# Kernel tuning notes

Hardware: AMD Instinct MI355X
Metric: run time of the kernel (lower is better)

Reference implementation:

```python
import jax, jax.numpy as jnp
import numpy as np

B, S, M, E, H, F, V, L = 2, 2048, 1024, 512, 8, 2048, 8192, 6


def setup_inputs() -> dict:
    key = jax.random.key(0)
    ks = iter(jax.random.split(key, 32))
    n = lambda shape, s=0.02: jax.random.normal(next(ks), shape, jnp.float32) * s
    return {
        "encoded": jax.random.normal(next(ks), (B, M, E), jnp.float32),
        "seq": jax.random.randint(next(ks), (B, S), 0, V, jnp.int32),
        "input_embed": n((V, E)),           # shared input/output embedding
        "pos_embed": n((S, E)),
        "output_bias": jnp.zeros((V,), jnp.float32),
        "self_in_w": n((L, 3 * E, E)), "self_in_b": jnp.zeros((L, 3 * E), jnp.float32),
        "self_out_w": n((L, E, E)), "self_out_b": jnp.zeros((L, E), jnp.float32),
        "cross_in_w": n((L, 3 * E, E)), "cross_in_b": jnp.zeros((L, 3 * E), jnp.float32),
        "cross_out_w": n((L, E, E)), "cross_out_b": jnp.zeros((L, E), jnp.float32),
        "self_norm_g": jnp.ones((L, E), jnp.float32), "self_norm_b": jnp.zeros((L, E), jnp.float32),
        "cross_norm_g": jnp.ones((L, E), jnp.float32), "cross_norm_b": jnp.zeros((L, E), jnp.float32),
        "mlp_norm_g": jnp.ones((L, E), jnp.float32), "mlp_norm_b": jnp.zeros((L, E), jnp.float32),
        "lin1_w": n((L, F, E)), "lin1_b": jnp.zeros((L, F), jnp.float32),
        "lin2_w": n((L, E, F)), "lin2_b": jnp.zeros((L, E), jnp.float32),
        "final_norm_g": jnp.ones((E,), jnp.float32), "final_norm_b": jnp.zeros((E,), jnp.float32),
    }


def _ln(x, g, b, eps=1e-5):
    m = jnp.mean(x, axis=-1, keepdims=True)
    v = jnp.mean((x - m) ** 2, axis=-1, keepdims=True)
    return (x - m) * jax.lax.rsqrt(v + eps) * g + b


def _mha(q, k, v, in_w, in_b, out_w, out_b, mask):
    # torch nn.MultiheadAttention (batch_first) with packed in_proj [3E, E]
    Ed = q.shape[-1]
    dh = Ed // H
    qp = q @ in_w[:Ed].T + in_b[:Ed]
    kp = k @ in_w[Ed:2 * Ed].T + in_b[Ed:2 * Ed]
    vp = v @ in_w[2 * Ed:].T + in_b[2 * Ed:]
    split = lambda t: t.reshape(t.shape[0], t.shape[1], H, dh).transpose(0, 2, 1, 3)
    qh, kh, vh = split(qp), split(kp), split(vp)  # [B, H, S, dh]
    scores = jnp.einsum('bhqd,bhkd->bhqk', qh, kh) / jnp.sqrt(jnp.float32(dh))
    if mask is not None:
        scores = jnp.where(mask, scores, jnp.float32(-1e9))
    attn = jax.nn.softmax(scores, axis=-1)
    o = jnp.einsum('bhqk,bhkd->bhqd', attn, vh)
    o = o.transpose(0, 2, 1, 3).reshape(q.shape[0], q.shape[1], Ed)
    return o @ out_w.T + out_b


def reference(encoded, seq, input_embed, pos_embed, output_bias,
              self_in_w, self_in_b, self_out_w, self_out_b,
              cross_in_w, cross_in_b, cross_out_w, cross_out_b,
              self_norm_g, self_norm_b, cross_norm_g, cross_norm_b,
              mlp_norm_g, mlp_norm_b, lin1_w, lin1_b, lin2_w, lin2_b,
              final_norm_g, final_norm_b):
    # TransformerDecoder.fit: teacher-forced forward (eval-mode dropout = identity)
    seq_len = seq.shape[1]
    x = input_embed[seq] + pos_embed[:seq_len]          # [B, S, E]
    causal = jnp.tril(jnp.ones((seq_len, seq_len), bool))
    for i in range(L):
        # post-norm decoder layer (norm_first=False)
        attn = _mha(x, x, x, self_in_w[i], self_in_b[i], self_out_w[i], self_out_b[i], causal)
        y = _ln(x + attn, self_norm_g[i], self_norm_b[i])
        cattn = _mha(y, encoded, encoded, cross_in_w[i], cross_in_b[i], cross_out_w[i], cross_out_b[i], None)
        y = _ln(y + cattn, cross_norm_g[i], cross_norm_b[i])
        h = jax.nn.gelu(y @ lin1_w[i].T + lin1_b[i], approximate=False)
        x = _ln(y + h @ lin2_w[i].T + lin2_b[i], mlp_norm_g[i], mlp_norm_b[i])
    x = _ln(x, final_norm_g, final_norm_b)               # decoder-final norm
    return x @ input_embed.T + output_bias               # shared output embedding
```

## Files before the change

### kernel.cpp

```cpp
#include <hip/hip_runtime.h>
#include <math.h>

typedef unsigned short u16;
typedef __attribute__((ext_vector_type(8))) unsigned short u16x8;
typedef __attribute__((ext_vector_type(8))) __bf16 bf16x8;
typedef __attribute__((ext_vector_type(4))) float f32x4;

constexpr int Bc = 2, Sc = 2048, Mc = 1024, Ec = 512, Hc = 8, DH = 64, Fc = 2048, Vc = 8192, Lc = 6;
constexpr int Nc = Bc * Sc;
constexpr int NMc = Bc * Mc;

__device__ __forceinline__ u16 f2b(float f) {
  __bf16 h = (__bf16)f;
  return __builtin_bit_cast(u16, h);
}
__device__ __forceinline__ float b2f_lo(unsigned w) { return __builtin_bit_cast(float, w << 16); }
__device__ __forceinline__ float b2f_hi(unsigned w) { return __builtin_bit_cast(float, w & 0xFFFF0000u); }

__device__ __forceinline__ f32x4 mfma16(bf16x8 a, bf16x8 b, f32x4 c) {
  return __builtin_amdgcn_mfma_f32_16x16x32_bf16(a, b, c, 0, 0, 0);
}

constexpr int C0 = 1179648;
constexpr int C1 = C0 + 393216;
constexpr int C2 = C1 + 1179648;
constexpr int C3 = C2 + 393216;
constexpr int C4 = C3 + 1572864;
constexpr int C5 = C4 + 1572864;
constexpr int C6 = C5 + 1048576;
constexpr int C7 = C6 + 262144;
constexpr int C8 = C7 + Nc * Ec / 4;

__global__ __launch_bounds__(256) void k_cvt_all(
    const float* __restrict__ s0, const float* __restrict__ s1,
    const float* __restrict__ s2, const float* __restrict__ s3,
    const float* __restrict__ s4, const float* __restrict__ s5,
    const float* __restrict__ s6, const float* __restrict__ s7,
    u16* __restrict__ d0, u16* __restrict__ d1, u16* __restrict__ d2,
    u16* __restrict__ d3, u16* __restrict__ d4, u16* __restrict__ d5,
    u16* __restrict__ d6, u16* __restrict__ d7,
    const int* __restrict__ seq, const float* __restrict__ pos,
    float* __restrict__ xs, u16* __restrict__ xb) {
  int i = blockIdx.x * 256 + threadIdx.x;
  if (i >= C7) {
    int j = i - C7;
    int idx0 = j * 4;
    int row = idx0 >> 9, e = idx0 & 511;
    int s = row & (Sc - 1);
    float4 ev = *(const float4*)(s6 + (size_t)seq[row] * Ec + e);
    float4 pv = *(const float4*)(pos + (size_t)s * Ec + e);
    float4 v = make_float4(ev.x + pv.x, ev.y + pv.y, ev.z + pv.z, ev.w + pv.w);
    ((float4*)xs)[j] = v;
    unsigned lo = (unsigned)f2b(v.x) | ((unsigned)f2b(v.y) << 16);
    unsigned hi = (unsigned)f2b(v.z) | ((unsigned)f2b(v.w) << 16);
    ((uint2*)xb)[j] = make_uint2(lo, hi);
    return;
  }
  const float* s; u16* d; int off;
  if (i < C3) {
    if (i < C1) { if (i < C0) { s = s0; d = d0; off = i; }
                  else        { s = s1; d = d1; off = i - C0; } }
    else        { if (i < C2) { s = s2; d = d2; off = i - C1; }
                  else        { s = s3; d = d3; off = i - C2; } }
  } else {
    if (i < C5) { if (i < C4) { s = s4; d = d4; off = i - C3; }
                  else        { s = s5; d = d5; off = i - C4; } }
    else        { if (i < C6) { s = s6; d = d6; off = i - C5; }
                  else        { s = s7; d = d7; off = i - C6; } }
  }
  float4 v = ((const float4*)s)[off];
  unsigned lo = (unsigned)f2b(v.x) | ((unsigned)f2b(v.y) << 16);
  unsigned hi = (unsigned)f2b(v.z) | ((unsigned)f2b(v.w) << 16);
  ((uint2*)d)[off] = make_uint2(lo, hi);
}

template <int BM, int BN, int ACT>
__device__ __forceinline__ void gemm_body(const u16* __restrict__ A,
                                          const u16* __restrict__ W,
                                          const float* __restrict__ bias,
                                          float* __restrict__ C32,
                                          u16* __restrict__ Cb,
                                          int K, int Mo,
                                          size_t row0, size_t col0) {
  constexpr int WM = BM / 2, WN = BN / 2, FM = WM / 16, FN = WN / 16;
  __shared__ __attribute__((aligned(16))) u16 As[2][BM * 64];
  __shared__ __attribute__((aligned(16))) u16 Bs[2][BN * 64];
  const int tid = threadIdx.x;
  const int w = tid >> 6, l = tid & 63, l15 = l & 15, l4 = l >> 4;
  const int lr = l >> 3, lc = l & 7;
  const int wr = (w >> 1) * WM, wc = (w & 1) * WN;
  const u16* Ab = A + row0 * K;
  const u16* Wb = W + col0 * K;
  f32x4 acc[FM][FN] = {};

  auto stage = [&](int buf, int k0) {
#pragma unroll
    for (int i = 0; i < BM / 32; ++i) {
      int sw = lr ^ ((i * 4 + w) & 7);
      int row = i * 32 + w * 8 + lr;
      const u16* ga = Ab + (size_t)row * K + k0 + ((lc ^ sw) & 7) * 8;
      __builtin_amdgcn_global_load_lds((const __attribute__((address_space(1))) void*)ga,
          (__attribute__((address_space(3))) void*)((char*)As[buf] + (i * 32 + w * 8) * 128), 16, 0, 0);
    }
#pragma unroll
    for (int i = 0; i < BN / 32; ++i) {
      int sw = lr ^ ((i * 4 + w) & 7);
      int row = i * 32 + w * 8 + lr;
      const u16* gw = Wb + (size_t)row * K + k0 + ((lc ^ sw) & 7) * 8;
      __builtin_amdgcn_global_load_lds((const __attribute__((address_space(1))) void*)gw,
          (__attribute__((address_space(3))) void*)((char*)Bs[buf] + (i * 32 + w * 8) * 128), 16, 0, 0);
    }
  };
  auto compute = [&](int buf) {
    const u16* AsC = As[buf];
    const u16* BsC = Bs[buf];
#pragma unroll
    for (int ks = 0; ks < 2; ++ks) {
      bf16x8 af[FM], bfr[FN];
#pragma unroll
      for (int m = 0; m < FM; ++m) {
        int ra = wr + m * 16 + l15;
        int sw = (l15 & 7) ^ ((wr / 8 + 2 * m + (l15 >> 3)) & 7);
        af[m] = *(const bf16x8*)&AsC[ra * 64 + ((ks * 32 + l4 * 8) ^ (sw * 8))];
      }
#pragma unroll
      for (int n = 0; n < FN; ++n) {
        int rb = wc + n * 16 + l15;
        int sw = (l15 & 7) ^ ((wc / 8 + 2 * n + (l15 >> 3)) & 7);
        bfr[n] = *(const bf16x8*)&BsC[rb * 64 + ((ks * 32 + l4 * 8) ^ (sw * 8))];
      }
#pragma unroll
      for (int m = 0; m < FM; ++m)
#pragma unroll
        for (int n = 0; n < FN; ++n)
          acc[m][n] = mfma16(af[m], bfr[n], acc[m][n]);
    }
  };

  const int nk = K / 64;
  stage(0, 0);
  int cur = 0;
  for (int kt = 0; kt < nk; ++kt) {
    __syncthreads();
    if (kt + 1 < nk) stage(cur ^ 1, (kt + 1) * 64);
    compute(cur);
    cur ^= 1;
  }

#pragma unroll
  for (int n = 0; n < FN; ++n) {
    size_t col = col0 + wc + n * 16 + l15;
    float bv = bias[col];
#pragma unroll
    for (int m = 0; m < FM; ++m)
#pragma unroll
      for (int r = 0; r < 4; ++r) {
        size_t row = row0 + wr + m * 16 + l4 * 4 + r;
        float v = acc[m][n][r] + bv;
        if (ACT) v = 0.5f * v * (1.f + erff(v * 0.70710678118654752f));
        if (C32) C32[row * Mo + col] = v;
        if (Cb) Cb[row * Mo + col] = f2b(v);
      }
  }
}

template <int BM, int BN, int ACT, int XS>
__global__ __launch_bounds__(256) void k_gemm_bf(const u16* __restrict__ A,
                                                 const u16* __restrict__ W,
                                                 const float* __restrict__ bias,
                                                 float* __restrict__ C32,
                                                 u16* __restrict__ Cb,
                                                 int K, int Mo) {
  int bx, by;
  if constexpr (XS) {
    int gx = gridDim.x;
    int bid = blockIdx.x + gx * blockIdx.y;
    int cw = gx >> 3;
    int xcd = bid & 7, j = bid >> 3;
    bx = xcd * cw + (j % cw);
    by = j / cw;
  } else {
    bx = blockIdx.x; by = blockIdx.y;
  }
  gemm_body<BM, BN, ACT>(A, W, bias, C32, Cb, K, Mo, (size_t)by * BM, (size_t)bx * BN);
}

__global__ __launch_bounds__(256) void k_gemm_cross(
    const u16* __restrict__ A0, const u16* __restrict__ W0, const float* __restrict__ b0,
    u16* __restrict__ Co0,
    const u16* __restrict__ A1, const u16* __restrict__ W1, const float* __restrict__ b1,
    u16* __restrict__ Co1) {
  int bid = blockIdx.x;
  if (bid < 512) {
    int xcd = bid & 7, j = bid >> 3;
    gemm_body<64, 64, 0>(A0, W0, b0, nullptr, Co0, Ec, Ec, (size_t)j * 64, (size_t)xcd * 64);
  } else {
    int r = bid - 512;
    int xcd = r & 7, j = r >> 3;
    int bx = xcd * 2 + (j & 1), by = j >> 1;
    gemm_body<64, 64, 0>(A1, W1, b1, nullptr, Co1, Ec, 2 * Ec, (size_t)by * 64, (size_t)bx * 64);
  }
}

__global__ __launch_bounds__(512, 4) void k_flash(const u16* __restrict__ Qp, int sq,
                                                  const u16* __restrict__ Kp,
                                                  const u16* __restrict__ Vp, int skv,
                                                  u16* __restrict__ Op, int so,
                                                  int Sq, int Sk, int causal) {
  __shared__ __attribute__((aligned(16))) u16 Kst[4][64 * 64];
  __shared__ __attribute__((aligned(16))) u16 Vt[4][64 * 64];
  __shared__ __attribute__((aligned(16))) u16 Pl[8][16 * 64];
  const int tid = threadIdx.x;
  const int w = tid >> 6, l = tid & 63, l15 = l & 15, l4 = l >> 4;
  const int wq = w & 3, ws = w >> 2;
  const int lr = l >> 3, lc = l & 7;
  const int t256 = tid & 255;
  const int kk2 = t256 >> 3, dblk = tid & 7;
  const int nqt = Sq / 64, nkt = Sk / 64;
  const int h = blockIdx.y, b = blockIdx.z;
  const int bx = blockIdx.x;
  const int qi = causal ? ((b & 1) ? bx : (nqt - 1 - bx)) : bx;
  const int qt0 = qi * 64;
  const int nt = causal ? (qi + 1) : nkt;
  const int NI = (nt + 1) >> 1;
  const u16* Qb = Qp + (size_t)b * Sq * sq + h * DH;
  const u16* Kb = Kp + (size_t)b * Sk * skv + h * DH;
  const u16* Vb = Vp + (size_t)b * Sk * skv + h * DH;
  const int qg = qt0 + wq * 16 + l15;

  bf16x8 qf[2];
  {
    const u16* qp0 = Qb + (size_t)qg * sq + l4 * 8;
    qf[0] = *(const bf16x8*)(qp0);
    qf[1] = *(const bf16x8*)(qp0 + 32);
  }

  f32x4 oacc[4] = {};
  float ls = 0.f, Mx = -3e38f;
  const float CSC = 0.18033688011112042f;
  const int swp = (l15 & 7) ^ (l15 >> 3);

  u16x8 va, vbv;
  auto stageK = [&](int slot, int kt) {
#pragma unroll
    for (int i = 0; i < 2; ++i) {
      int sw = lr ^ ((i * 4 + wq) & 7);
      int row = i * 32 + wq * 8 + lr;
      const u16* src = Kb + (size_t)(kt + row) * skv + ((lc ^ sw) & 7) * 8;
      __builtin_amdgcn_global_load_lds((const __attribute__((address_space(1))) void*)src,
          (__attribute__((address_space(3))) void*)((char*)Kst[slot] + (i * 32 + wq * 8) * 128), 16, 0, 0);
    }
  };
  auto loadV = [&](int kt) {
    const u16* vp0 = Vb + (size_t)(kt + 2 * kk2) * skv + dblk * 8;
    va = *(const u16x8*)vp0;
    vbv = *(const u16x8*)(vp0 + skv);
  };
  auto writeV = [&](int slot) {
    char* Vb_ = (char*)Vt[slot];
#pragma unroll
    for (int j = 0; j < 8; ++j) {
      int d = dblk * 8 + j;
      int sw = (j ^ dblk) & 7;
      unsigned pk = (unsigned)va[j] | ((unsigned)vbv[j] << 16);
      *(unsigned*)(Vb_ + d * 128 + ((4 * kk2) ^ (sw << 4))) = pk;
    }
  };

  stageK(ws * 2, ws * 64);
  loadV(ws * 64);
  writeV(ws * 2);
  asm volatile("s_waitcnt lgkmcnt(0)" ::: "memory");
  __builtin_amdgcn_sched_barrier(0);
  __builtin_amdgcn_s_barrier();

  u16* Pw = Pl[w];
  for (int i = 0; i < NI; ++i) {
    const int t = 2 * i + ws;
    const int tn = t + 2;
    const int cur = ws * 2 + (i & 1);
    const int nxt = ws * 2 + ((i + 1) & 1);
    const bool haveNext = tn < nt;
    if (haveNext) {
      stageK(nxt, tn * 64);
      loadV(tn * 64);
    }
    if (t < nt) {
      const u16* KstC = Kst[cur];
      const u16* VtC = Vt[cur];

      f32x4 sf[4] = {};
      __builtin_amdgcn_s_setprio(1);
#pragma unroll
      for (int n = 0; n < 4; ++n) {
        int rk = n * 16 + l15;
        int sw = (l15 & 7) ^ ((2 * n + (l15 >> 3)) & 7);
#pragma unroll
        for (int ks = 0; ks < 2; ++ks) {
          bf16x8 kf = *(const bf16x8*)&KstC[rk * 64 + ((ks * 32 + l4 * 8) ^ (sw * 8))];
          sf[n] = mfma16(kf, qf[ks], sf[n]);
        }
      }
      __builtin_amdgcn_s_setprio(0);

      if (causal && t == nt - 1) {
#pragma unroll
        for (int n = 0; n < 4; ++n)
#pragma unroll
          for (int r = 0; r < 4; ++r) {
            int kcol = t * 64 + n * 16 + l4 * 4 + r;
            if (kcol > qg) sf[n][r] = -3e38f;
          }
      }

      float tm = fmaxf(fmaxf(fmaxf(sf[0][0], sf[0][1]), fmaxf(sf[0][2], sf[0][3])),
                       fmaxf(fmaxf(sf[1][0], sf[1][1]), fmaxf(sf[1][2], sf[1][3])));
      tm = fmaxf(tm, fmaxf(fmaxf(fmaxf(sf[2][0], sf[2][1]), fmaxf(sf[2][2], sf[2][3])),
                           fmaxf(fmaxf(sf[3][0], sf[3][1]), fmaxf(sf[3][2], sf[3][3]))));
      tm = fmaxf(tm, __shfl_xor(tm, 16, 64));
      tm = fmaxf(tm, __shfl_xor(tm, 32, 64));
      float Mn = fmaxf(Mx, tm);
      float al = exp2f((Mx - Mn) * CSC);
      Mx = Mn;
      float mxc = Mx * CSC;

      float rs = 0.f;
#pragma unroll
      for (int n = 0; n < 4; ++n) {
        float p0 = exp2f(sf[n][0] * CSC - mxc);
        float p1 = exp2f(sf[n][1] * CSC - mxc);
        float p2 = exp2f(sf[n][2] * CSC - mxc);
        float p3 = exp2f(sf[n][3] * CSC - mxc);
        rs += (p0 + p1) + (p2 + p3);
        unsigned w0 = (unsigned)f2b(p0) | ((unsigned)f2b(p1) << 16);
        unsigned w1 = (unsigned)f2b(p2) | ((unsigned)f2b(p3) << 16);
        int bb = (n * 32 + l4 * 8) ^ (swp << 4);
        *(unsigned*)((char*)Pw + l15 * 128 + bb) = w0;
        *(unsigned*)((char*)Pw + l15 * 128 + bb + 4) = w1;
      }
      rs += __shfl_xor(rs, 16, 64);
      rs += __shfl_xor(rs, 32, 64);
      ls = ls * al + rs;

      if (__any(al < 1.f)) {
        float a0 = __shfl(al, l4 * 4 + 0, 64);
        float a1 = __shfl(al, l4 * 4 + 1, 64);
        float a2 = __shfl(al, l4 * 4 + 2, 64);
        float a3 = __shfl(al, l4 * 4 + 3, 64);
#pragma unroll
        for (int n2 = 0; n2 < 4; ++n2) {
          oacc[n2][0] *= a0; oacc[n2][1] *= a1;
          oacc[n2][2] *= a2; oacc[n2][3] *= a3;
        }
      }

      asm volatile("s_waitcnt lgkmcnt(0)" ::: "memory");
      __builtin_amdgcn_sched_barrier(0);

      __builtin_amdgcn_s_setprio(1);
#pragma unroll
      for (int ks = 0; ks < 2; ++ks) {
        bf16x8 pf = *(const bf16x8*)((char*)Pw + l15 * 128 + ((ks * 64 + l4 * 16) ^ (swp << 4)));
#pragma unroll
        for (int n2 = 0; n2 < 4; ++n2) {
          int rd = n2 * 16 + l15;
          int sw = (l15 & 7) ^ ((2 * n2 + (l15 >> 3)) & 7);
          bf16x8 vf = *(const bf16x8*)((char*)VtC + rd * 128 + ((ks * 64 + l4 * 16) ^ (sw << 4)));
          oacc[n2] = mfma16(pf, vf, oacc[n2]);
        }
      }
      __builtin_amdgcn_s_setprio(0);
    }

    if (haveNext) writeV(nxt);
    asm volatile("s_waitcnt lgkmcnt(0)" ::: "memory");
    __builtin_amdgcn_sched_barrier(0);
    __builtin_amdgcn_s_barrier();
  }

  __syncthreads();
  float* OB = (float*)&Kst[0][0];
  float* ML = (float*)&Vt[0][0];
  if (l4 == 0) {
    ML[ws * 64 + wq * 16 + l15] = Mx;
    ML[128 + ws * 64 + wq * 16 + l15] = ls;
  }
  if (ws == 1) {
#pragma unroll
    for (int n2 = 0; n2 < 4; ++n2)
#pragma unroll
      for (int r = 0; r < 4; ++r)
        OB[(wq * 16 + l4 * 4 + r) * 64 + n2 * 16 + l15] = oacc[n2][r];
  }
  __syncthreads();
  if (ws == 0) {
    u16* Ob = Op + (size_t)b * Sq * so + h * DH;
#pragma unroll
    for (int r = 0; r < 4; ++r) {
      int qs = wq * 16 + l4 * 4 + r;
      float mA = ML[qs], mB = ML[64 + qs];
      float lA = ML[128 + qs], lB = ML[192 + qs];
      float M = fmaxf(mA, mB);
      float aA = exp2f((mA - M) * CSC);
      float aB = exp2f((mB - M) * CSC);
      float inv = 1.f / (lA * aA + lB * aB);
      int qrow = qt0 + qs;
#pragma unroll
      for (int n2 = 0; n2 < 4; ++n2) {
        float o = (oacc[n2][r] * aA + OB[qs * 64 + n2 * 16 + l15] * aB) * inv;
        Ob[(size_t)qrow * so + n2 * 16 + l15] = f2b(o);
      }
    }
  }
}

__global__ __launch_bounds__(256) void k_res_ln(const float* __restrict__ xin,
                                                const u16* __restrict__ rres,
                                                const float* __restrict__ g,
                                                const float* __restrict__ bet,
                                                float* __restrict__ outf,
                                                u16* __restrict__ outb,
                                                int has_res) {
  const int tid = threadIdx.x, w = tid >> 6, l = tid & 63;
  const int row = blockIdx.x * 4 + w;
  const float4* xr = (const float4*)(xin + (size_t)row * Ec);
  float4 a = xr[2 * l], c = xr[2 * l + 1];
  if (has_res) {
    uint4 rv = ((const uint4*)(rres + (size_t)row * Ec))[l];
    a.x += b2f_lo(rv.x); a.y += b2f_hi(rv.x);
    a.z += b2f_lo(rv.y); a.w += b2f_hi(rv.y);
    c.x += b2f_lo(rv.z); c.y += b2f_hi(rv.z);
    c.z += b2f_lo(rv.w); c.w += b2f_hi(rv.w);
  }
  float s = (a.x + a.y) + (a.z + a.w) + (c.x + c.y) + (c.z + c.w);
#pragma unroll
  for (int o = 32; o; o >>= 1) s += __shfl_xor(s, o, 64);
  const float mean = s * (1.f / Ec);
  float d0 = a.x - mean, d1 = a.y - mean, d2 = a.z - mean, d3 = a.w - mean;
  float e0 = c.x - mean, e1 = c.y - mean, e2 = c.z - mean, e3 = c.w - mean;
  float vs = d0 * d0 + d1 * d1 + d2 * d2 + d3 * d3 +
             e0 * e0 + e1 * e1 + e2 * e2 + e3 * e3;
#pragma unroll
  for (int o = 32; o; o >>= 1) vs += __shfl_xor(vs, o, 64);
  const float inv = rsqrtf(vs * (1.f / Ec) + 1e-5f);
  float4 g0 = ((const float4*)g)[2 * l], g1 = ((const float4*)g)[2 * l + 1];
  float4 b0 = ((const float4*)bet)[2 * l], b1 = ((const float4*)bet)[2 * l + 1];
  float o0 = d0 * inv * g0.x + b0.x, o1 = d1 * inv * g0.y + b0.y;
  float o2 = d2 * inv * g0.z + b0.z, o3 = d3 * inv * g0.w + b0.w;
  float o4 = e0 * inv * g1.x + b1.x, o5 = e1 * inv * g1.y + b1.y;
  float o6 = e2 * inv * g1.z + b1.z, o7 = e3 * inv * g1.w + b1.w;
  if (outf) {
    float4* orow = (float4*)(outf + (size_t)row * Ec);
    orow[2 * l] = make_float4(o0, o1, o2, o3);
    orow[2 * l + 1] = make_float4(o4, o5, o6, o7);
  }
  if (outb) {
    uint4 pk;
    pk.x = (unsigned)f2b(o0) | ((unsigned)f2b(o1) << 16);
    pk.y = (unsigned)f2b(o2) | ((unsigned)f2b(o3) << 16);
    pk.z = (unsigned)f2b(o4) | ((unsigned)f2b(o5) << 16);
    pk.w = (unsigned)f2b(o6) | ((unsigned)f2b(o7) << 16);
    ((uint4*)(outb + (size_t)row * Ec))[l] = pk;
  }
}

extern "C" void kernel_launch(void* const* d_in, const int* in_sizes, int n_in,
                              void* d_out, int out_size, void* d_ws, size_t ws_size,
                              hipStream_t stream) {
  const float* encoded      = (const float*)d_in[0];
  const int*   seq          = (const int*)d_in[1];
  const float* input_embed  = (const float*)d_in[2];
  const float* pos_embed    = (const float*)d_in[3];
  const float* output_bias  = (const float*)d_in[4];
  const float* self_in_w    = (const float*)d_in[5];
  const float* self_in_b    = (const float*)d_in[6];
  const float* self_out_w   = (const float*)d_in[7];
  const float* self_out_b   = (const float*)d_in[8];
  const float* cross_in_w   = (const float*)d_in[9];
  const float* cross_in_b   = (const float*)d_in[10];
  const float* cross_out_w  = (const float*)d_in[11];
  const float* cross_out_b  = (const float*)d_in[12];
  const float* self_norm_g  = (const float*)d_in[13];
  const float* self_norm_b  = (const float*)d_in[14];
  const float* cross_norm_g = (const float*)d_in[15];
  const float* cross_norm_b = (const float*)d_in[16];
  const float* mlp_norm_g   = (const float*)d_in[17];
  const float* mlp_norm_b   = (const float*)d_in[18];
  const float* lin1_w       = (const float*)d_in[19];
  const float* lin1_b       = (const float*)d_in[20];
  const float* lin2_w       = (const float*)d_in[21];
  const float* lin2_b       = (const float*)d_in[22];
  const float* final_norm_g = (const float*)d_in[23];
  const float* final_norm_b = (const float*)d_in[24];

  char* oc = (char*)d_out;
  auto take = [&](size_t bytes) { char* p = oc; oc += bytes; return p; };
  u16* wsi  = (u16*)take((size_t)Lc * 3 * Ec * Ec * 2);
  u16* wso  = (u16*)take((size_t)Lc * Ec * Ec * 2);
  u16* wci  = (u16*)take((size_t)Lc * 3 * Ec * Ec * 2);
  u16* wco  = (u16*)take((size_t)Lc * Ec * Ec * 2);
  u16* wl1  = (u16*)take((size_t)Lc * Fc * Ec * 2);
  u16* wl2  = (u16*)take((size_t)Lc * Ec * Fc * 2);
  u16* encb = (u16*)take((size_t)NMc * Ec * 2);
  float* xs  = (float*)take((size_t)Nc * Ec * 4);
  float* ys  = (float*)take((size_t)Nc * Ec * 4);
  u16* tmpb = (u16*)take((size_t)Nc * Ec * 2);
  u16* xbf  = (u16*)take((size_t)Nc * Ec * 2);
  u16* qkvb = (u16*)take((size_t)Nc * 3 * Ec * 2);
  u16* ctxb = (u16*)take((size_t)Nc * Ec * 2);
  u16* qxb  = (u16*)take((size_t)Nc * Ec * 2);
  u16* kvb  = (u16*)take((size_t)NMc * 2 * Ec * 2);
  u16* hbf  = (u16*)take((size_t)Nc * Fc * 2);
  u16* xfb  = (u16*)d_ws;
  u16* embb = (u16*)((char*)d_ws + (size_t)Nc * Ec * 2);

  const dim3 blk(256);
  k_cvt_all<<<dim3(C8 / 256), blk, 0, stream>>>(
      self_in_w, self_out_w, cross_in_w, cross_out_w, lin1_w, lin2_w,
      input_embed, encoded, wsi, wso, wci, wco, wl1, wl2, embb, encb,
      seq, pos_embed, xs, xbf);

  const dim3 gAttn(Sc / 64, Hc, Bc);
  const dim3 blkA(512);
  const dim3 gLN(Nc / 4);
  for (int l = 0; l < Lc; ++l) {
    const u16* wsi_l = wsi + (size_t)l * 3 * Ec * Ec;
    const u16* wci_l = wci + (size_t)l * 3 * Ec * Ec;
    k_gemm_bf<128, 64, 0, 1><<<dim3(3 * Ec / 64, Nc / 128), blk, 0, stream>>>(
        xbf, wsi_l, self_in_b + (size_t)l * 3 * Ec, nullptr, qkvb, Ec, 3 * Ec);
    k_flash<<<gAttn, blkA, 0, stream>>>(qkvb, 3 * Ec, qkvb + Ec, qkvb + 2 * Ec, 3 * Ec,
                                        ctxb, Ec, Sc, Sc, 1);
    k_gemm_bf<64, 64, 0, 1><<<dim3(Ec / 64, Nc / 64), blk, 0, stream>>>(
        ctxb, wso + (size_t)l * Ec * Ec, self_out_b + (size_t)l * Ec, nullptr, tmpb, Ec, Ec);
    k_res_ln<<<gLN, blk, 0, stream>>>(xs, tmpb, self_norm_g + (size_t)l * Ec,
                                      self_norm_b + (size_t)l * Ec, ys, xbf, 1);
    k_gemm_cross<<<dim3(1024), blk, 0, stream>>>(
        xbf, wci_l, cross_in_b + (size_t)l * 3 * Ec, qxb,
        encb, wci_l + (size_t)Ec * Ec, cross_in_b + (size_t)l * 3 * Ec + Ec, kvb);
    k_flash<<<gAttn, blkA, 0, stream>>>(qxb, Ec, kvb, kvb + Ec, 2 * Ec,
                                        ctxb, Ec, Sc, Mc, 0);
    k_gemm_bf<64, 64, 0, 1><<<dim3(Ec / 64, Nc / 64), blk, 0, stream>>>(
        ctxb, wco + (size_t)l * Ec * Ec, cross_out_b + (size_t)l * Ec, nullptr, tmpb, Ec, Ec);
    k_res_ln<<<gLN, blk, 0, stream>>>(ys, tmpb, cross_norm_g + (size_t)l * Ec,
                                      cross_norm_b + (size_t)l * Ec, xs, xbf, 1);
    k_gemm_bf<128, 128, 1, 1><<<dim3(Fc / 128, Nc / 128), blk, 0, stream>>>(
        xbf, wl1 + (size_t)l * Fc * Ec, lin1_b + (size_t)l * Fc, nullptr, hbf, Ec, Fc);
    k_gemm_bf<64, 64, 0, 1><<<dim3(Ec / 64, Nc / 64), blk, 0, stream>>>(
        hbf, wl2 + (size_t)l * Ec * Fc, lin2_b + (size_t)l * Ec, nullptr, tmpb, Fc, Ec);
    k_res_ln<<<gLN, blk, 0, stream>>>(xs, tmpb, mlp_norm_g + (size_t)l * Ec,
                                      mlp_norm_b + (size_t)l * Ec, xs, xbf, 1);
  }

  k_res_ln<<<gLN, blk, 0, stream>>>(xs, nullptr, final_norm_g, final_norm_b, nullptr, xfb, 0);
  k_gemm_bf<128, 128, 0, 1><<<dim3(Vc / 128, Nc / 128), blk, 0, stream>>>(
      xfb, embb, output_bias, (float*)d_out, nullptr, Ec, Vc);
}
```

Before: 1.124 ms.

## Hoist cross-attention KV projection for all layers and split-K the lin2 GEMM

The encoder K/V projection depends only on the encoded input, so it is now computed once for all six layers in a single up-front launch into a per-layer KV buffer. The per-layer cross GEMM then only projects Q. The lin2 GEMM (K=2048) is split into two K halves that run as 1024 blocks writing separate partial outputs, and the residual LayerNorm sums both partials. This trades extra memory (six KV buffers, a second temp buffer) and an extra partial read for more parallelism in the under-occupied lin2 launch. hbf now aliases qkvb to save space.

```diff
diff --git a/kernel.cpp b/kernel.cpp
--- a/kernel.cpp
+++ b/kernel.cpp
@@ -80,7 +80,7 @@
                                           const float* __restrict__ bias,
                                           float* __restrict__ C32,
                                           u16* __restrict__ Cb,
-                                          int K, int Mo,
+                                          int K, int lda, int ldw, int Mo,
                                           size_t row0, size_t col0) {
   constexpr int WM = BM / 2, WN = BN / 2, FM = WM / 16, FN = WN / 16;
   __shared__ __attribute__((aligned(16))) u16 As[2][BM * 64];
@@ -89,8 +89,8 @@
   const int w = tid >> 6, l = tid & 63, l15 = l & 15, l4 = l >> 4;
   const int lr = l >> 3, lc = l & 7;
   const int wr = (w >> 1) * WM, wc = (w & 1) * WN;
-  const u16* Ab = A + row0 * K;
-  const u16* Wb = W + col0 * K;
+  const u16* Ab = A + row0 * lda;
+  const u16* Wb = W + col0 * ldw;
   f32x4 acc[FM][FN] = {};
 
   auto stage = [&](int buf, int k0) {
@@ -98,7 +98,7 @@
     for (int i = 0; i < BM / 32; ++i) {
       int sw = lr ^ ((i * 4 + w) & 7);
       int row = i * 32 + w * 8 + lr;
-      const u16* ga = Ab + (size_t)row * K + k0 + ((lc ^ sw) & 7) * 8;
+      const u16* ga = Ab + (size_t)row * lda + k0 + ((lc ^ sw) & 7) * 8;
       __builtin_amdgcn_global_load_lds((const __attribute__((address_space(1))) void*)ga,
           (__attribute__((address_space(3))) void*)((char*)As[buf] + (i * 32 + w * 8) * 128), 16, 0, 0);
     }
@@ -106,7 +106,7 @@
     for (int i = 0; i < BN / 32; ++i) {
       int sw = lr ^ ((i * 4 + w) & 7);
       int row = i * 32 + w * 8 + lr;
-      const u16* gw = Wb + (size_t)row * K + k0 + ((lc ^ sw) & 7) * 8;
+      const u16* gw = Wb + (size_t)row * ldw + k0 + ((lc ^ sw) & 7) * 8;
       __builtin_amdgcn_global_load_lds((const __attribute__((address_space(1))) void*)gw,
           (__attribute__((address_space(3))) void*)((char*)Bs[buf] + (i * 32 + w * 8) * 128), 16, 0, 0);
     }
@@ -150,7 +150,7 @@
 #pragma unroll
   for (int n = 0; n < FN; ++n) {
     size_t col = col0 + wc + n * 16 + l15;
-    float bv = bias[col];
+    float bv = bias ? bias[col] : 0.f;
 #pragma unroll
     for (int m = 0; m < FM; ++m)
 #pragma unroll
@@ -182,24 +182,36 @@
   } else {
     bx = blockIdx.x; by = blockIdx.y;
   }
-  gemm_body<BM, BN, ACT>(A, W, bias, C32, Cb, K, Mo, (size_t)by * BM, (size_t)bx * BN);
-}
-
-__global__ __launch_bounds__(256) void k_gemm_cross(
-    const u16* __restrict__ A0, const u16* __restrict__ W0, const float* __restrict__ b0,
-    u16* __restrict__ Co0,
-    const u16* __restrict__ A1, const u16* __restrict__ W1, const float* __restrict__ b1,
-    u16* __restrict__ Co1) {
+  gemm_body<BM, BN, ACT>(A, W, bias, C32, Cb, K, K, K, Mo, (size_t)by * BM, (size_t)bx * BN);
+}
+
+__global__ __launch_bounds__(256) void k_gemm_kv(const u16* __restrict__ encb,
+                                                 const u16* __restrict__ wci,
+                                                 const float* __restrict__ cib,
+                                                 u16* __restrict__ kvb) {
   int bid = blockIdx.x;
-  if (bid < 512) {
-    int xcd = bid & 7, j = bid >> 3;
-    gemm_body<64, 64, 0>(A0, W0, b0, nullptr, Co0, Ec, Ec, (size_t)j * 64, (size_t)xcd * 64);
-  } else {
-    int r = bid - 512;
-    int xcd = r & 7, j = r >> 3;
-    int bx = xcd * 2 + (j & 1), by = j >> 1;
-    gemm_body<64, 64, 0>(A1, W1, b1, nullptr, Co1, Ec, 2 * Ec, (size_t)by * 64, (size_t)bx * 64);
-  }
+  int lay = bid >> 9, r = bid & 511;
+  int xcd = r & 7, j = r >> 3;
+  int bx = xcd * 2 + (j & 1), by = j >> 1;
+  const u16* W = wci + (size_t)lay * 3 * Ec * Ec + (size_t)Ec * Ec;
+  const float* b = cib + (size_t)lay * 3 * Ec + Ec;
+  u16* out = kvb + (size_t)lay * NMc * 2 * Ec;
+  gemm_body<64, 64, 0>(encb, W, b, nullptr, out, Ec, Ec, Ec, 2 * Ec,
+                       (size_t)by * 64, (size_t)bx * 64);
+}
+
+__global__ __launch_bounds__(256) void k_gemm_lin2(const u16* __restrict__ hbf,
+                                                   const u16* __restrict__ wl2_l,
+                                                   const float* __restrict__ bias,
+                                                   u16* __restrict__ t0,
+                                                   u16* __restrict__ t1) {
+  int bid = blockIdx.x;
+  int half = bid >> 9, r = bid & 511;
+  int xcd = r & 7, j = r >> 3;
+  const u16* A = hbf + half * 1024;
+  const u16* W = wl2_l + half * 1024;
+  gemm_body<64, 64, 0>(A, W, half ? nullptr : bias, nullptr, half ? t1 : t0,
+                       1024, Fc, Fc, Ec, (size_t)j * 64, (size_t)xcd * 64);
 }
 
 __global__ __launch_bounds__(512, 4) void k_flash(const u16* __restrict__ Qp, int sq,
@@ -416,6 +428,7 @@
 
 __global__ __launch_bounds__(256) void k_res_ln(const float* __restrict__ xin,
                                                 const u16* __restrict__ rres,
+                                                const u16* __restrict__ rres2,
                                                 const float* __restrict__ g,
                                                 const float* __restrict__ bet,
                                                 float* __restrict__ outf,
@@ -431,6 +444,13 @@
     a.z += b2f_lo(rv.y); a.w += b2f_hi(rv.y);
     c.x += b2f_lo(rv.z); c.y += b2f_hi(rv.z);
     c.z += b2f_lo(rv.w); c.w += b2f_hi(rv.w);
+    if (rres2) {
+      uint4 r2 = ((const uint4*)(rres2 + (size_t)row * Ec))[l];
+      a.x += b2f_lo(r2.x); a.y += b2f_hi(r2.x);
+      a.z += b2f_lo(r2.y); a.w += b2f_hi(r2.y);
+      c.x += b2f_lo(r2.z); c.y += b2f_hi(r2.z);
+      c.z += b2f_lo(r2.w); c.w += b2f_hi(r2.w);
+    }
   }
   float s = (a.x + a.y) + (a.z + a.w) + (c.x + c.y) + (c.z + c.w);
 #pragma unroll
@@ -504,13 +524,14 @@
   u16* encb = (u16*)take((size_t)NMc * Ec * 2);
   float* xs  = (float*)take((size_t)Nc * Ec * 4);
   float* ys  = (float*)take((size_t)Nc * Ec * 4);
-  u16* tmpb = (u16*)take((size_t)Nc * Ec * 2);
+  u16* tmpb  = (u16*)take((size_t)Nc * Ec * 2);
+  u16* tmpb2 = (u16*)take((size_t)Nc * Ec * 2);
   u16* xbf  = (u16*)take((size_t)Nc * Ec * 2);
   u16* qkvb = (u16*)take((size_t)Nc * 3 * Ec * 2);
   u16* ctxb = (u16*)take((size_t)Nc * Ec * 2);
   u16* qxb  = (u16*)take((size_t)Nc * Ec * 2);
-  u16* kvb  = (u16*)take((size_t)NMc * 2 * Ec * 2);
-  u16* hbf  = (u16*)take((size_t)Nc * Fc * 2);
+  u16* kvb  = (u16*)take((size_t)Lc * NMc * 2 * Ec * 2);
+  u16* hbf  = qkvb;
   u16* xfb  = (u16*)d_ws;
   u16* embb = (u16*)((char*)d_ws + (size_t)Nc * Ec * 2);
 
@@ -519,6 +540,8 @@
       self_in_w, self_out_w, cross_in_w, cross_out_w, lin1_w, lin2_w,
       input_embed, encoded, wsi, wso, wci, wco, wl1, wl2, embb, encb,
       seq, pos_embed, xs, xbf);
+
+  k_gemm_kv<<<dim3(Lc * 512), blk, 0, stream>>>(encb, wci, cross_in_b, kvb);
 
   const dim3 gAttn(Sc / 64, Hc, Bc);
   const dim3 blkA(512);
@@ -526,32 +549,33 @@
   for (int l = 0; l < Lc; ++l) {
     const u16* wsi_l = wsi + (size_t)l * 3 * Ec * Ec;
     const u16* wci_l = wci + (size_t)l * 3 * Ec * Ec;
+    u16* kvb_l = kvb + (size_t)l * NMc * 2 * Ec;
     k_gemm_bf<128, 64, 0, 1><<<dim3(3 * Ec / 64, Nc / 128), blk, 0, stream>>>(
         xbf, wsi_l, self_in_b + (size_t)l * 3 * Ec, nullptr, qkvb, Ec, 3 * Ec);
     k_flash<<<gAttn, blkA, 0, stream>>>(qkvb, 3 * Ec, qkvb + Ec, qkvb + 2 * Ec, 3 * Ec,
                                         ctxb, Ec, Sc, Sc, 1);
     k_gemm_bf<64, 64, 0, 1><<<dim3(Ec / 64, Nc / 64), blk, 0, stream>>>(
         ctxb, wso + (size_t)l * Ec * Ec, self_out_b + (size_t)l * Ec, nullptr, tmpb, Ec, Ec);
-    k_res_ln<<<gLN, blk, 0, stream>>>(xs, tmpb, self_norm_g + (size_t)l * Ec,
+    k_res_ln<<<gLN, blk, 0, stream>>>(xs, tmpb, nullptr, self_norm_g + (size_t)l * Ec,
                                       self_norm_b + (size_t)l * Ec, ys, xbf, 1);
-    k_gemm_cross<<<dim3(1024), blk, 0, stream>>>(
-        xbf, wci_l, cross_in_b + (size_t)l * 3 * Ec, qxb,
-        encb, wci_l + (size_t)Ec * Ec, cross_in_b + (size_t)l * 3 * Ec + Ec, kvb);
-    k_flash<<<gAttn, blkA, 0, stream>>>(qxb, Ec, kvb, kvb + Ec, 2 * Ec,
+    k_gemm_bf<64, 64, 0, 1><<<dim3(Ec / 64, Nc / 64), blk, 0, stream>>>(
+        xbf, wci_l, cross_in_b + (size_t)l * 3 * Ec, nullptr, qxb, Ec, Ec);
+    k_flash<<<gAttn, blkA, 0, stream>>>(qxb, Ec, kvb_l, kvb_l + Ec, 2 * Ec,
                                         ctxb, Ec, Sc, Mc, 0);
     k_gemm_bf<64, 64, 0, 1><<<dim3(Ec / 64, Nc / 64), blk, 0, stream>>>(
         ctxb, wco + (size_t)l * Ec * Ec, cross_out_b + (size_t)l * Ec, nullptr, tmpb, Ec, Ec);
-    k_res_ln<<<gLN, blk, 0, stream>>>(ys, tmpb, cross_norm_g + (size_t)l * Ec,
+    k_res_ln<<<gLN, blk, 0, stream>>>(ys, tmpb, nullptr, cross_norm_g + (size_t)l * Ec,
                                       cross_norm_b + (size_t)l * Ec, xs, xbf, 1);
     k_gemm_bf<128, 128, 1, 1><<<dim3(Fc / 128, Nc / 128), blk, 0, stream>>>(
         xbf, wl1 + (size_t)l * Fc * Ec, lin1_b + (size_t)l * Fc, nullptr, hbf, Ec, Fc);
-    k_gemm_bf<64, 64, 0, 1><<<dim3(Ec / 64, Nc / 64), blk, 0, stream>>>(
-        hbf, wl2 + (size_t)l * Ec * Fc, lin2_b + (size_t)l * Ec, nullptr, tmpb, Fc, Ec);
-    k_res_ln<<<gLN, blk, 0, stream>>>(xs, tmpb, mlp_norm_g + (size_t)l * Ec,
+    k_gemm_lin2<<<dim3(1024), blk, 0, stream>>>(
+        hbf, wl2 + (size_t)l * Ec * Fc, lin2_b + (size_t)l * Ec, tmpb, tmpb2);
+    k_res_ln<<<gLN, blk, 0, stream>>>(xs, tmpb, tmpb2, mlp_norm_g + (size_t)l * Ec,
                                       mlp_norm_b + (size_t)l * Ec, xs, xbf, 1);
   }
 
-  k_res_ln<<<gLN, blk, 0, stream>>>(xs, nullptr, final_norm_g, final_norm_b, nullptr, xfb, 0);
+  k_res_ln<<<gLN, blk, 0, stream>>>(xs, nullptr, nullptr, final_norm_g, final_norm_b,
+                                    nullptr, xfb, 0);
   k_gemm_bf<128, 128, 0, 1><<<dim3(Vc / 128, Nc / 128), blk, 0, stream>>>(
       xfb, embb, output_bias, (float*)d_out, nullptr, Ec, Vc);
 }
```

Result: no change. 1.126 ms (+0.2%).
